# Optimization experiments

Hardware: AMD Instinct MI355X
Metric: run time of the kernel (lower is better)

The kernel has to match this reference:

```python
import jax, jax.numpy as jnp
import numpy as np

EPS = 1e-5
B, T, D, V, NB, C, R, MT = 2, 256, 2048, 32000, 4, 512, 32, 3


def ste_sign_vec(w):
    alpha = jnp.mean(jnp.abs(w))
    hard = alpha * jnp.sign(w)
    hard = jnp.where(hard == 0, alpha, hard)
    return w + jax.lax.stop_gradient(hard - w)


def ste_sign(w):
    alpha = jnp.mean(jnp.abs(w), axis=-1, keepdims=True)
    hard = alpha * jnp.sign(w)
    hard = jnp.where(hard == 0, alpha, hard)
    return w + jax.lax.stop_gradient(hard - w)


def layernorm(x, g, b):
    m = jnp.mean(x, axis=-1, keepdims=True)
    v = jnp.var(x, axis=-1, keepdims=True)
    return (x - m) * jax.lax.rsqrt(v + EPS) * g + b


def hdc_block(x, i, decay_logit, bv_q, bv_k, bv_v, rules, query_bind, logic_gate,
              ln_mem_g, ln_mem_b, ln_attn_g, ln_attn_b, ln_logic_g, ln_logic_b,
              ctrl_ln_g, ctrl_ln_b, down_w, down_b, up_w, up_b):
    t = jnp.arange(T)
    # --- EMA memory (conv1d with decay^k kernel == lower-tri decay matmul) ---
    decay = jax.nn.sigmoid(decay_logit[i])
    expnt = t[:, None] - t[None, :]                     # (T,T)
    A = jnp.where(expnt >= 0, decay ** jnp.maximum(expnt, 0).astype(x.dtype), 0.0)
    mem = jnp.einsum('ts,bsd->btd', A, x)
    x = layernorm(x + mem, ln_mem_g[i], ln_mem_b[i])
    # --- sigmoid-gated boolean causal attention ---
    Q = x * ste_sign_vec(bv_q[i])
    K = x * ste_sign_vec(bv_k[i])
    Vv = x * ste_sign_vec(bv_v[i])
    scores = jnp.einsum('btd,bsd->bts', Q, K) * (D ** -0.5)
    causal = t[:, None] >= t[None, :]
    attn = jnp.where(causal[None], jax.nn.sigmoid(scores * 4.0), 0.0)
    att_out = jnp.einsum('bts,bsd->btd', attn, Vv)
    x = layernorm(x + att_out, ln_attn_g[i], ln_attn_b[i])
    # --- logic layer: sum_r w_r * (x*rule_r) == x * (w @ rules) ---
    rls = ste_sign(rules[i])                            # (R,D)
    query = x * ste_sign_vec(query_bind[i])
    sim = jnp.einsum('btd,rd->btr', query, rls) * (D ** -0.5)
    rw = jax.nn.sigmoid(sim * 4.0)
    logic_out = x * jnp.einsum('btr,rd->btd', rw, rls)
    gate = jax.nn.sigmoid(logic_gate[i])
    x = layernorm(x + gate * (logic_out - x), ln_logic_g[i], ln_logic_b[i])
    # --- controller MLP (dropout inactive in eval) ---
    h = layernorm(x, ctrl_ln_g[i], ctrl_ln_b[i])
    h = jax.nn.gelu(h @ down_w[i].T + down_b[i], approximate=False)
    h = h @ up_w[i].T + up_b[i]
    return x + h


def setup_inputs() -> dict:
    key = jax.random.key(0)
    ks = jax.random.split(key, 12)
    nrm = jax.random.normal
    return {
        'idx': jax.random.randint(ks[0], (B, T), 0, V),
        'codebook': 0.02 * nrm(ks[1], (V, D)),
        'decay_logit': jnp.full((NB,), 2.0),
        'bv_q': 0.5 * nrm(ks[2], (NB, D)),
        'bv_k': 0.5 * nrm(ks[3], (NB, D)),
        'bv_v': 0.5 * nrm(ks[4], (NB, D)),
        'rules': 0.5 * nrm(ks[5], (NB, R, D)),
        'query_bind': 0.5 * nrm(ks[6], (NB, D)),
        'logic_gate': jnp.full((NB,), -1.0),
        'ln_mem_g': jnp.ones((NB, D)), 'ln_mem_b': jnp.zeros((NB, D)),
        'ln_attn_g': jnp.ones((NB, D)), 'ln_attn_b': jnp.zeros((NB, D)),
        'ln_logic_g': jnp.ones((NB, D)), 'ln_logic_b': jnp.zeros((NB, D)),
        'ctrl_ln_g': jnp.ones((NB, D)), 'ctrl_ln_b': jnp.zeros((NB, D)),
        'down_w': nrm(ks[7], (NB, C, D)) / np.sqrt(D), 'down_b': jnp.zeros((NB, C)),
        'up_w': nrm(ks[8], (NB, D, C)) / np.sqrt(C), 'up_b': jnp.zeros((NB, D)),
        'tl_gates': jnp.zeros((MT,)),
        'tl_pos': 0.01 * nrm(ks[9], (MT, D)),
        'tl_ln_g': jnp.ones((D,)), 'tl_ln_b': jnp.zeros((D,)),
        'out_ln_g': jnp.ones((D,)), 'out_ln_b': jnp.zeros((D,)),
        'output_scale': jnp.array(1.0),
    }


def reference(idx, codebook, decay_logit, bv_q, bv_k, bv_v, rules, query_bind,
              logic_gate, ln_mem_g, ln_mem_b, ln_attn_g, ln_attn_b, ln_logic_g,
              ln_logic_b, ctrl_ln_g, ctrl_ln_b, down_w, down_b, up_w, up_b,
              tl_gates, tl_pos, tl_ln_g, tl_ln_b, out_ln_g, out_ln_b, output_scale):
    blk = (decay_logit, bv_q, bv_k, bv_v, rules, query_bind, logic_gate,
           ln_mem_g, ln_mem_b, ln_attn_g, ln_attn_b, ln_logic_g, ln_logic_b,
           ctrl_ln_g, ctrl_ln_b, down_w, down_b, up_w, up_b)

    def run_blocks(h):
        for i in range(NB):
            h = hdc_block(h, i, *blk)
        return h

    # encode: STE bipolar codebook + cyclic permutation positional binding
    tokens = ste_sign(jnp.take(codebook, idx, axis=0))  # (B,T,D)
    perm = (jnp.arange(D)[None, :] - jnp.arange(T)[:, None]) % D  # (T,D)
    tokens = jnp.take_along_axis(tokens, jnp.broadcast_to(perm[None], tokens.shape), axis=2)

    h = run_blocks(tokens)
    for ti in range(1, MT):  # thought loop (n_thoughts = max_thoughts)
        gate = jax.nn.sigmoid(tl_gates[ti])
        thought = run_blocks(layernorm(h, tl_ln_g, tl_ln_b) + tl_pos[ti])
        h = h + gate * (thought - h)

    h = layernorm(h, out_ln_g, out_ln_b)
    logits = (h @ codebook.T) * output_scale  # (B,T,V) weight-tied decoder
    return logits
```

## Files before the change

kernel.cpp:

```cpp
#include <hip/hip_runtime.h>
#include <math.h>

#define TT   256
#define DD   2048
#define VV   32000
#define NBLK 4
#define CC   512
#define RR   32
#define MTT  3
#define NBAT 2
#define NTOK 512

typedef unsigned int u32;
typedef unsigned short ushort_t;
typedef __attribute__((ext_vector_type(8))) short s16x8;
typedef __attribute__((ext_vector_type(4))) float f32x4;

__device__ __forceinline__ float sigm(float x){ return 1.0f/(1.0f+expf(-x)); }

__device__ __forceinline__ ushort_t f2bf(float f){
  u32 u = __float_as_uint(f);
  u32 r = (u + 0x7fffu + ((u >> 16) & 1u)) >> 16;
  return (ushort_t)r;
}
__device__ __forceinline__ float bf2f(ushort_t u){
  return __uint_as_float(((u32)u) << 16);
}

__device__ __forceinline__ void async_copy16(void* lds, const void* g){
  __builtin_amdgcn_global_load_lds((const __attribute__((address_space(1))) u32*)g,
                                   (__attribute__((address_space(3))) u32*)lds, 16, 0, 0);
}

__device__ __forceinline__ float block_sum256(float v){
  #pragma unroll
  for (int off = 32; off > 0; off >>= 1) v += __shfl_down(v, off);
  __shared__ float sh[4];
  __syncthreads();
  if ((threadIdx.x & 63) == 0) sh[threadIdx.x >> 6] = v;
  __syncthreads();
  return sh[0] + sh[1] + sh[2] + sh[3];
}

__global__ __launch_bounds__(256) void cvt2_kernel(const float* __restrict__ a,
    ushort_t* __restrict__ oa, long na4,
    const float* __restrict__ b, ushort_t* __restrict__ ob, long nb4){
  long i = (long)blockIdx.x * 256 + threadIdx.x;
  long stride = (long)gridDim.x * 256;
  long tot = na4 + nb4;
  for (; i < tot; i += stride){
    const float* src = (i < na4) ? a : b;
    ushort_t* dst = (i < na4) ? oa : ob;
    long k = (i < na4) ? i : i - na4;
    float4 v = ((const float4*)src)[k];
    ushort4 o;
    o.x = f2bf(v.x); o.y = f2bf(v.y); o.z = f2bf(v.z); o.w = f2bf(v.w);
    ((ushort4*)dst)[k] = o;
  }
}

__global__ __launch_bounds__(256) void sign_prep_kernel(
    const float* __restrict__ bv_q, const float* __restrict__ bv_k,
    const float* __restrict__ bv_v, const float* __restrict__ query_bind,
    const float* __restrict__ rules,
    float* __restrict__ SQK, float* __restrict__ SV, float* __restrict__ SQB,
    ushort_t* __restrict__ RLSb){
  int b = blockIdx.x;
  if (b < NBLK){
    const float* q = bv_q + (size_t)b * DD;
    const float* k = bv_k + (size_t)b * DD;
    float sq = 0.f, sk = 0.f;
    #pragma unroll
    for (int j = 0; j < 8; j++){
      int d = threadIdx.x + j*256;
      sq += fabsf(q[d]); sk += fabsf(k[d]);
    }
    float aq = block_sum256(sq) * (1.f/DD);
    float ak = block_sum256(sk) * (1.f/DD);
    float a2 = aq * ak;
    float* o = SQK + (size_t)b * DD;
    #pragma unroll
    for (int j = 0; j < 8; j++){
      int d = threadIdx.x + j*256;
      o[d] = ((q[d] < 0.f) != (k[d] < 0.f)) ? -a2 : a2;
    }
    return;
  }
  const float* w; float* of = nullptr; ushort_t* ob = nullptr;
  if (b < 2*NBLK){ w = bv_v + (size_t)(b - NBLK) * DD; of = SV + (size_t)(b - NBLK) * DD; }
  else if (b < 3*NBLK){ w = query_bind + (size_t)(b - 2*NBLK) * DD; of = SQB + (size_t)(b - 2*NBLK) * DD; }
  else { int r = b - 3*NBLK; w = rules + (size_t)r * DD; ob = RLSb + (size_t)r * DD; }
  float s = 0.f;
  #pragma unroll
  for (int j = 0; j < 8; j++) s += fabsf(w[threadIdx.x + j*256]);
  float a = block_sum256(s) * (1.f/DD);
  #pragma unroll
  for (int j = 0; j < 8; j++){
    int d = threadIdx.x + j*256;
    float v = (w[d] < 0.f) ? -a : a;
    if (of) of[d] = v;
    else    ob[d] = f2bf(v);
  }
}

__global__ __launch_bounds__(256) void encode_kernel(const int* __restrict__ idx,
    const float* __restrict__ cb, float* __restrict__ X, ushort_t* __restrict__ Xrb){
  int token = blockIdx.x;
  int t = token & (TT - 1);
  size_t row = (size_t)idx[token] * DD;
  float s = 0.f;
  #pragma unroll
  for (int j = 0; j < 8; j++) s += fabsf(cb[row + threadIdx.x + j*256]);
  float a = block_sum256(s) * (1.f/DD);
  #pragma unroll
  for (int j = 0; j < 8; j++){
    int d = threadIdx.x + j*256;
    float w = cb[row + ((d - t) & (DD - 1))];
    float v = (w < 0.f) ? -a : a;
    X[(size_t)token * DD + d] = v;
    Xrb[(size_t)token * DD + d] = f2bf(v);
  }
}

__global__ __launch_bounds__(256) void adec_kernel(const float* __restrict__ decay_logit,
    ushort_t* __restrict__ Adec){
  int i = blockIdx.y, t = blockIdx.x, s = threadIdx.x;
  float decay = sigm(decay_logit[i]);
  float l2 = log2f(decay);
  int e = t - s;
  float v = (e < 0) ? 0.f : exp2f((float)e * l2);
  Adec[((size_t)i*TT + t)*TT + s] = f2bf(v);
}

__global__ __launch_bounds__(256) void ln_kernel(const float* __restrict__ A,
    const float* __restrict__ g, const float* __restrict__ be,
    float* __restrict__ out, ushort_t* __restrict__ outb,
    const float* __restrict__ qscale, ushort_t* __restrict__ outq,
    const float* __restrict__ vscale, ushort_t* __restrict__ outv){
  size_t row = blockIdx.x;
  const float* a = A + row * DD;
  float vals[8]; float s = 0.f, ss = 0.f;
  #pragma unroll
  for (int j = 0; j < 8; j++){
    int d = threadIdx.x + j*256;
    float v = a[d];
    vals[j] = v; s += v; ss += v*v;
  }
  float mean = block_sum256(s) * (1.f/DD);
  float var  = block_sum256(ss) * (1.f/DD) - mean*mean;
  float inv  = rsqrtf(var + 1e-5f);
  #pragma unroll
  for (int j = 0; j < 8; j++){
    int d = threadIdx.x + j*256;
    float y = (vals[j] - mean) * inv * g[d] + be[d];
    if (out)  out[row*DD + d] = y;
    if (outb) outb[row*DD + d] = f2bf(y);
    if (outq) outq[row*DD + d] = f2bf(y * qscale[d]);
    if (outv) outv[row*DD + d] = f2bf(y * vscale[d]);
  }
}

__global__ __launch_bounds__(256) void fuse_logic_kernel(const float* __restrict__ T0,
    const ushort_t* __restrict__ RLSi, const float* __restrict__ SQBi,
    const float* __restrict__ g2, const float* __restrict__ b2,
    const float* __restrict__ gate_ptr,
    const float* __restrict__ g3, const float* __restrict__ b3,
    const float* __restrict__ g4, const float* __restrict__ b4,
    float* __restrict__ X, ushort_t* __restrict__ T1b){
  __shared__ float sh[256*33];
  __shared__ float red[8*32];
  __shared__ float rwsh[32];
  const float RSD = 0.022097086912079608f;
  int tid = threadIdx.x;
  size_t tok = blockIdx.x;
  const float* a = T0 + tok * DD;
  float v[8]; float s = 0.f, ss = 0.f;
  #pragma unroll
  for (int j = 0; j < 8; j++){
    int d = tid + 256*j;
    v[j] = a[d]; s += v[j]; ss += v[j]*v[j];
  }
  float mean = block_sum256(s) * (1.f/DD);
  float var  = block_sum256(ss) * (1.f/DD) - mean*mean;
  float inv  = rsqrtf(var + 1e-5f);
  float y2[8], xq[8];
  #pragma unroll
  for (int j = 0; j < 8; j++){
    int d = tid + 256*j;
    y2[j] = (v[j] - mean) * inv * g2[d] + b2[d];
    xq[j] = y2[j] * SQBi[d];
  }
  float aa[32];
  #pragma unroll 4
  for (int r = 0; r < 32; r++){
    float t = 0.f;
    #pragma unroll
    for (int j = 0; j < 8; j++)
      t = fmaf(xq[j], bf2f(RLSi[(size_t)r*DD + tid + 256*j]), t);
    aa[r] = t;
  }
  #pragma unroll
  for (int r = 0; r < 32; r++) sh[tid*33 + r] = aa[r];
  __syncthreads();
  {
    int r = tid & 31, gg = tid >> 5;
    float t = 0.f;
    #pragma unroll 8
    for (int i = 0; i < 32; i++) t += sh[(gg*32 + i)*33 + r];
    red[gg*32 + r] = t;
  }
  __syncthreads();
  if (tid < 32){
    float t = 0.f;
    #pragma unroll
    for (int gg = 0; gg < 8; gg++) t += red[gg*32 + tid];
    rwsh[tid] = sigm(4.f * RSD * t);
  }
  __syncthreads();
  float gate = sigm(*gate_ptr);
  float p3[8]; s = 0.f; ss = 0.f;
  #pragma unroll
  for (int j = 0; j < 8; j++){
    int d = tid + 256*j;
    float t = 0.f;
    #pragma unroll 8
    for (int r = 0; r < 32; r++)
      t = fmaf(rwsh[r], bf2f(RLSi[(size_t)r*DD + d]), t);
    float lo = y2[j] * t;
    p3[j] = y2[j] + gate * (lo - y2[j]);
    s += p3[j]; ss += p3[j]*p3[j];
  }
  mean = block_sum256(s) * (1.f/DD);
  var  = block_sum256(ss) * (1.f/DD) - mean*mean;
  inv  = rsqrtf(var + 1e-5f);
  float y3[8]; s = 0.f; ss = 0.f;
  #pragma unroll
  for (int j = 0; j < 8; j++){
    int d = tid + 256*j;
    y3[j] = (p3[j] - mean) * inv * g3[d] + b3[d];
    X[tok*DD + d] = y3[j];
    s += y3[j]; ss += y3[j]*y3[j];
  }
  mean = block_sum256(s) * (1.f/DD);
  var  = block_sum256(ss) * (1.f/DD) - mean*mean;
  inv  = rsqrtf(var + 1e-5f);
  #pragma unroll
  for (int j = 0; j < 8; j++){
    int d = tid + 256*j;
    T1b[tok*DD + d] = f2bf((y3[j] - mean) * inv * g4[d] + b4[d]);
  }
}

__global__ __launch_bounds__(256) void tl_kernel(const float* __restrict__ Xr,
    float* __restrict__ H, const float* __restrict__ gate_ptr,
    const float* __restrict__ g, const float* __restrict__ be,
    const float* __restrict__ pos,
    float* __restrict__ outX, ushort_t* __restrict__ outXb){
  size_t row = blockIdx.x;
  float gate = gate_ptr ? sigm(*gate_ptr) : 1.f;
  float v[8]; float s = 0.f, ss = 0.f;
  #pragma unroll
  for (int j = 0; j < 8; j++){
    int d = threadIdx.x + j*256;
    float xr = Xr[row*DD + d];
    float hv = gate_ptr ? H[row*DD + d] : 0.f;
    float hn = gate_ptr ? (hv + gate * (xr - hv)) : xr;
    H[row*DD + d] = hn;
    v[j] = hn; s += hn; ss += hn*hn;
  }
  float mean = block_sum256(s) * (1.f/DD);
  float var  = block_sum256(ss) * (1.f/DD) - mean*mean;
  float inv  = rsqrtf(var + 1e-5f);
  #pragma unroll
  for (int j = 0; j < 8; j++){
    int d = threadIdx.x + j*256;
    float y = (v[j] - mean) * inv * g[d] + be[d];
    if (pos) y += pos[d];
    if (outX)  outX[row*DD + d] = y;
    if (outXb) outXb[row*DD + d] = f2bf(y);
  }
}

template<int BM, int BN, int SPLITK, int ACT, bool CAUSAL, bool OUTBF>
__global__ __launch_bounds__(256) void gemm_nt(const ushort_t* __restrict__ A,
    const ushort_t* __restrict__ B, void* __restrict__ Cv,
    int K, int lda, int ldb, int ldc,
    long sA, long sB, long sC,
    const float* __restrict__ colscale, const float* __restrict__ bias,
    const float* __restrict__ res, ushort_t* __restrict__ mirror,
    const float* __restrict__ alpha_ptr, float alpha_c)
{
  constexpr int FM = BM / 32;
  constexpr int FN = BN / 32;
  __shared__ __align__(16) ushort_t shA[BM * 64];
  __shared__ __align__(16) ushort_t shB[BN * 64];
  const int tid = threadIdx.x;
  const int l = tid & 63, w = tid >> 6;
  const int wr = w >> 1, wc = w & 1;
  const int row0 = blockIdx.y * BM, col0 = blockIdx.x * BN;
  const int zb = blockIdx.z / SPLITK, zk = blockIdx.z % SPLITK;

  if (CAUSAL && col0 > row0 + BM - 1) return;

  A += (size_t)zb * sA;
  B += (size_t)zb * sB;
  const int kbeg = zk * (K / SPLITK), kend = kbeg + K / SPLITK;

  f32x4 acc[FM][FN] = {};

  for (int kt = kbeg; kt < kend; kt += 64){
    #pragma unroll
    for (int i = 0; i < BM/32; i++){
      int o = i*4096 + tid*16;
      int r = o >> 7, c = (o >> 4) & 7;
      int lc = c ^ (r & 7);
      async_copy16((char*)shA + o, A + (size_t)(row0 + r) * lda + kt + lc*8);
    }
    #pragma unroll
    for (int i = 0; i < BN/32; i++){
      int o = i*4096 + tid*16;
      int r = o >> 7, c = (o >> 4) & 7;
      int lc = c ^ (r & 7);
      async_copy16((char*)shB + o, B + (size_t)(col0 + r) * ldb + kt + lc*8);
    }
    __syncthreads();
    #pragma unroll
    for (int kk = 0; kk < 2; kk++){
      s16x8 af[FM], bfr[FN];
      #pragma unroll
      for (int mi = 0; mi < FM; mi++){
        int r = wr*(BM/2) + mi*16 + (l & 15);
        int c = kk*4 + (l >> 4);
        af[mi] = *(const s16x8*)((const char*)shA + r*128 + (c ^ (r & 7))*16);
      }
      #pragma unroll
      for (int ni = 0; ni < FN; ni++){
        int r = wc*(BN/2) + ni*16 + (l & 15);
        int c = kk*4 + (l >> 4);
        bfr[ni] = *(const s16x8*)((const char*)shB + r*128 + (c ^ (r & 7))*16);
      }
      #pragma unroll
      for (int mi = 0; mi < FM; mi++)
        #pragma unroll
        for (int ni = 0; ni < FN; ni++)
          acc[mi][ni] = __builtin_amdgcn_mfma_f32_16x16x32_bf16(af[mi], bfr[ni], acc[mi][ni], 0, 0, 0);
    }
    __syncthreads();
  }

  if (SPLITK > 1){
    float* P = (float*)Cv + (size_t)blockIdx.z * sC;
    #pragma unroll
    for (int mi = 0; mi < FM; mi++)
      #pragma unroll
      for (int ni = 0; ni < FN; ni++)
        #pragma unroll
        for (int j = 0; j < 4; j++){
          int m = row0 + wr*(BM/2) + mi*16 + (l >> 4)*4 + j;
          int n = col0 + wc*(BN/2) + ni*16 + (l & 15);
          P[(size_t)m * ldc + n] = acc[mi][ni][j];
        }
    return;
  }

  float alpha = alpha_c * (alpha_ptr ? *alpha_ptr : 1.f);
  float* Cf = (float*)Cv + (size_t)zb * sC;
  ushort_t* Cb = (ushort_t*)Cv + (size_t)zb * sC;
  const float* resz = res ? res + (size_t)zb * sC : nullptr;
  #pragma unroll
  for (int mi = 0; mi < FM; mi++){
    #pragma unroll
    for (int ni = 0; ni < FN; ni++){
      #pragma unroll
      for (int j = 0; j < 4; j++){
        int m = row0 + wr*(BM/2) + mi*16 + (l >> 4)*4 + j;
        int n = col0 + wc*(BN/2) + ni*16 + (l & 15);
        float v = acc[mi][ni][j] * alpha;
        if (colscale) v *= colscale[n];
        if (bias) v += bias[n];
        if (ACT == 1) v = sigm(4.f * v);
        else if (ACT == 2) v = 0.5f * v * (1.f + erff(v * 0.70710678118654752f));
        if (CAUSAL && n > m) v = 0.f;
        if (resz) v += resz[(size_t)m * ldc + n];
        if (OUTBF) Cb[(size_t)m * ldc + n] = f2bf(v);
        else       Cf[(size_t)m * ldc + n] = v;
        if (mirror) mirror[(size_t)m * ldc + n] = f2bf(v);
      }
    }
  }
}

__global__ __launch_bounds__(256) void gemm_nn(const ushort_t* __restrict__ A,
    const ushort_t* __restrict__ B, float* __restrict__ C,
    int K, int lda, int ldb, int ldc,
    long sA, long sB, long sC,
    const float* __restrict__ res)
{
  __shared__ __align__(16) ushort_t shA[64 * 64];
  __shared__ __align__(16) ushort_t shB[64 * 64];
  const int tid = threadIdx.x;
  const int l = tid & 63, w = tid >> 6;
  const int wr = w >> 1, wc = w & 1;
  const int row0 = blockIdx.y * 64, col0 = blockIdx.x * 64;
  A += (size_t)blockIdx.z * sA;
  B += (size_t)blockIdx.z * sB;

  const int kb = tid & 63;
  const int nb0 = (tid >> 6) * 8;

  f32x4 acc[2][2] = {};

  for (int kt = 0; kt < K; kt += 64){
    #pragma unroll
    for (int i = 0; i < 2; i++){
      int o = i*4096 + tid*16;
      int r = o >> 7, c = (o >> 4) & 7;
      int lc = c ^ (r & 7);
      async_copy16((char*)shA + o, A + (size_t)(row0 + r) * lda + kt + lc*8);
    }
    #pragma unroll
    for (int i = 0; i < 2; i++){
      int n0 = nb0 + i*32;
      s16x8 v = *(const s16x8*)(B + (size_t)(kt + kb) * ldb + col0 + n0);
      #pragma unroll
      for (int j = 0; j < 8; j++){
        int n = n0 + j;
        int off = n*128 + (((kb >> 3) ^ (n & 7)) << 4) + ((kb & 7) << 1);
        *(ushort_t*)((char*)shB + off) = (ushort_t)v[j];
      }
    }
    __syncthreads();
    #pragma unroll
    for (int kk = 0; kk < 2; kk++){
      s16x8 af[2], bfr[2];
      #pragma unroll
      for (int mi = 0; mi < 2; mi++){
        int r = wr*32 + mi*16 + (l & 15);
        int c = kk*4 + (l >> 4);
        af[mi] = *(const s16x8*)((const char*)shA + r*128 + ((c ^ (r & 7)) << 4));
      }
      #pragma unroll
      for (int ni = 0; ni < 2; ni++){
        int r = wc*32 + ni*16 + (l & 15);
        int c = kk*4 + (l >> 4);
        bfr[ni] = *(const s16x8*)((const char*)shB + r*128 + ((c ^ (r & 7)) << 4));
      }
      #pragma unroll
      for (int mi = 0; mi < 2; mi++)
        #pragma unroll
        for (int ni = 0; ni < 2; ni++)
          acc[mi][ni] = __builtin_amdgcn_mfma_f32_16x16x32_bf16(af[mi], bfr[ni], acc[mi][ni], 0, 0, 0);
    }
    __syncthreads();
  }

  float* Cf = C + (size_t)blockIdx.z * sC;
  const float* resz = res ? res + (size_t)blockIdx.z * sC : nullptr;
  #pragma unroll
  for (int mi = 0; mi < 2; mi++)
    #pragma unroll
    for (int ni = 0; ni < 2; ni++)
      #pragma unroll
      for (int j = 0; j < 4; j++){
        int m = row0 + wr*32 + mi*16 + (l >> 4)*4 + j;
        int n = col0 + wc*32 + ni*16 + (l & 15);
        float v = acc[mi][ni][j];
        if (resz) v += resz[(size_t)m * ldc + n];
        Cf[(size_t)m * ldc + n] = v;
      }
}

__global__ __launch_bounds__(256) void gemm_ntf(const ushort_t* __restrict__ A,
    const float* __restrict__ B, float* __restrict__ C,
    int K, int lda, int ldb, int ldc,
    const float* __restrict__ alpha_ptr)
{
  constexpr int BM = 256, BN = 64, FM = 8, FN = 2;
  __shared__ __align__(16) ushort_t shA[BM * 64];
  __shared__ __align__(16) ushort_t shB[BN * 64];
  const int tid = threadIdx.x;
  const int l = tid & 63, w = tid >> 6;
  const int wr = w >> 1, wc = w & 1;
  const int row0 = blockIdx.y * BM, col0 = blockIdx.x * BN;

  f32x4 acc[FM][FN] = {};

  for (int kt = 0; kt < K; kt += 64){
    #pragma unroll
    for (int i = 0; i < BM/32; i++){
      int o = i*4096 + tid*16;
      int r = o >> 7, c = (o >> 4) & 7;
      int lc = c ^ (r & 7);
      async_copy16((char*)shA + o, A + (size_t)(row0 + r) * lda + kt + lc*8);
    }
    #pragma unroll
    for (int i = 0; i < 4; i++){
      int c2 = tid + i*256;
      int r = c2 & 63, kq = c2 >> 6;
      float4 v = *(const float4*)(B + (size_t)(col0 + r) * ldb + kt + kq*4);
      u32 p0 = ((u32)f2bf(v.y) << 16) | (u32)f2bf(v.x);
      u32 p1 = ((u32)f2bf(v.w) << 16) | (u32)f2bf(v.z);
      int off = r*128 + (((kq >> 1) ^ (r & 7)) << 4) + ((kq & 1) << 3);
      uint2 pp; pp.x = p0; pp.y = p1;
      *(uint2*)((char*)shB + off) = pp;
    }
    __syncthreads();
    #pragma unroll
    for (int kk = 0; kk < 2; kk++){
      s16x8 af[FM], bfr[FN];
      #pragma unroll
      for (int mi = 0; mi < FM; mi++){
        int r = wr*(BM/2) + mi*16 + (l & 15);
        int c = kk*4 + (l >> 4);
        af[mi] = *(const s16x8*)((const char*)shA + r*128 + ((c ^ (r & 7)) << 4));
      }
      #pragma unroll
      for (int ni = 0; ni < FN; ni++){
        int r = wc*(BN/2) + ni*16 + (l & 15);
        int c = kk*4 + (l >> 4);
        bfr[ni] = *(const s16x8*)((const char*)shB + r*128 + ((c ^ (r & 7)) << 4));
      }
      #pragma unroll
      for (int mi = 0; mi < FM; mi++)
        #pragma unroll
        for (int ni = 0; ni < FN; ni++)
          acc[mi][ni] = __builtin_amdgcn_mfma_f32_16x16x32_bf16(af[mi], bfr[ni], acc[mi][ni], 0, 0, 0);
    }
    __syncthreads();
  }

  float alpha = *alpha_ptr;
  #pragma unroll
  for (int mi = 0; mi < FM; mi++)
    #pragma unroll
    for (int ni = 0; ni < FN; ni++)
      #pragma unroll
      for (int j = 0; j < 4; j++){
        int m = row0 + wr*(BM/2) + mi*16 + (l >> 4)*4 + j;
        int n = col0 + wc*(BN/2) + ni*16 + (l & 15);
        C[(size_t)m * ldc + n] = acc[mi][ni][j] * alpha;
      }
}

template<int S, int ACT, bool CAUSAL, bool OUTBF>
__global__ __launch_bounds__(256) void reduce_epi(const float* __restrict__ P,
    void* __restrict__ outv, int M, int N, const float* __restrict__ bias, float alpha){
  long MN = (long)M * N;
  long idx = ((long)blockIdx.x * 256 + threadIdx.x) * 4;
  int b = (int)(idx / MN);
  long r = idx - (long)b * MN;
  int m = (int)(r / N), n = (int)(r % N);
  float vv[4] = {0.f, 0.f, 0.f, 0.f};
  #pragma unroll
  for (int s = 0; s < S; s++){
    float4 p = *(const float4*)&P[((long)(b*S + s)) * MN + r];
    vv[0] += p.x; vv[1] += p.y; vv[2] += p.z; vv[3] += p.w;
  }
  ushort4 ob; float4 of;
  float* po = (float*)&of;
  ushort_t* pb = (ushort_t*)&ob;
  #pragma unroll
  for (int j = 0; j < 4; j++){
    float v = vv[j] * alpha;
    if (bias) v += bias[n + j];
    if (ACT == 1) v = sigm(4.f * v);
    else if (ACT == 2) v = 0.5f * v * (1.f + erff(v * 0.70710678118654752f));
    if (CAUSAL && n + j > m) v = 0.f;
    po[j] = v; pb[j] = f2bf(v);
  }
  if (OUTBF) *(ushort4*)&((ushort_t*)outv)[(long)b*MN + r] = ob;
  else       *(float4*)&((float*)outv)[(long)b*MN + r] = of;
}

extern "C" void kernel_launch(void* const* d_in, const int* in_sizes, int n_in,
                              void* d_out, int out_size, void* d_ws, size_t ws_size,
                              hipStream_t stream){
  const int*   idx        = (const int*)  d_in[0];
  const float* cb         = (const float*)d_in[1];
  const float* decay_lg   = (const float*)d_in[2];
  const float* bv_q       = (const float*)d_in[3];
  const float* bv_k       = (const float*)d_in[4];
  const float* bv_v       = (const float*)d_in[5];
  const float* rules      = (const float*)d_in[6];
  const float* query_bind = (const float*)d_in[7];
  const float* logic_gate = (const float*)d_in[8];
  const float* ln_mem_g   = (const float*)d_in[9];
  const float* ln_mem_b   = (const float*)d_in[10];
  const float* ln_attn_g  = (const float*)d_in[11];
  const float* ln_attn_b  = (const float*)d_in[12];
  const float* ln_logic_g = (const float*)d_in[13];
  const float* ln_logic_b = (const float*)d_in[14];
  const float* ctrl_g     = (const float*)d_in[15];
  const float* ctrl_b     = (const float*)d_in[16];
  const float* down_w     = (const float*)d_in[17];
  const float* down_b     = (const float*)d_in[18];
  const float* up_w       = (const float*)d_in[19];
  const float* up_b       = (const float*)d_in[20];
  const float* tl_gates   = (const float*)d_in[21];
  const float* tl_pos     = (const float*)d_in[22];
  const float* tl_g       = (const float*)d_in[23];
  const float* tl_b       = (const float*)d_in[24];
  const float* out_g      = (const float*)d_in[25];
  const float* out_b      = (const float*)d_in[26];
  const float* oscale     = (const float*)d_in[27];
  float* out = (float*)d_out;

  const size_t ND = (size_t)NTOK * DD;
  char* p = (char*)d_ws;
  auto alloc = [&](size_t bytes){ void* r = p; p += (bytes + 255) & ~(size_t)255; return r; };
  float*    X       = (float*)   alloc(ND * 4);
  float*    H       = (float*)   alloc(ND * 4);
  float*    T0      = (float*)   alloc(ND * 4);
  ushort_t* Xrb     = (ushort_t*)alloc(ND * 2);
  ushort_t* Xb      = (ushort_t*)alloc(ND * 2);
  ushort_t* Xqb     = (ushort_t*)alloc(ND * 2);
  ushort_t* Xvb     = (ushort_t*)alloc(ND * 2);
  ushort_t* T1b     = (ushort_t*)alloc(ND * 2);
  ushort_t* ATTNb   = (ushort_t*)alloc((size_t)NBAT * TT * TT * 2);
  ushort_t* CBb     = (ushort_t*)alloc((size_t)NTOK * CC * 2);
  float*    PP      = (float*)   alloc((size_t)8 * NTOK * CC * 4);
  float*    SQK     = (float*)   alloc((size_t)NBLK * DD * 4);
  float*    SV      = (float*)   alloc((size_t)NBLK * DD * 4);
  float*    SQB     = (float*)   alloc((size_t)NBLK * DD * 4);
  ushort_t* RLSb    = (ushort_t*)alloc((size_t)NBLK * RR * DD * 2);
  ushort_t* Adec    = (ushort_t*)alloc((size_t)NBLK * TT * TT * 2);
  ushort_t* down_wb = (ushort_t*)alloc((size_t)NBLK * CC * DD * 2);
  ushort_t* up_wb   = (ushort_t*)alloc((size_t)NBLK * DD * CC * 2);

  const float RSD = 0.022097086912079608f;

  sign_prep_kernel<<<3*NBLK + NBLK*RR, 256, 0, stream>>>(
      bv_q, bv_k, bv_v, query_bind, rules, SQK, SV, SQB, RLSb);
  adec_kernel<<<dim3(TT, NBLK), 256, 0, stream>>>(decay_lg, Adec);
  cvt2_kernel<<<2048, 256, 0, stream>>>(down_w, down_wb, (long)NBLK*CC*DD/4,
                                        up_w, up_wb, (long)NBLK*DD*CC/4);
  encode_kernel<<<NTOK, 256, 0, stream>>>(idx, cb, X, Xrb);

  auto run_blocks = [&](){
    for (int i = 0; i < NBLK; i++){
      const size_t iD = (size_t)i * DD;
      gemm_nn<<<dim3(DD/64, TT/64, NBAT), 256, 0, stream>>>(
          Adec + (size_t)i*TT*TT, Xrb, T0, TT, TT, DD, DD,
          0, (long)TT*DD, (long)TT*DD, X);
      ln_kernel<<<NTOK, 256, 0, stream>>>(T0, ln_mem_g + iD, ln_mem_b + iD,
          X, Xb, SQK + iD, Xqb, SV + iD, Xvb);
      gemm_nt<64,64,8,0,true,false><<<dim3(TT/64, TT/64, NBAT*8), 256, 0, stream>>>(
          Xqb, Xb, PP, DD, DD, DD, TT,
          (long)TT*DD, (long)TT*DD, (long)TT*TT,
          nullptr, nullptr, nullptr, nullptr, nullptr, 1.f);
      reduce_epi<8,1,true,true><<<(NBAT*TT*TT)/1024, 256, 0, stream>>>(
          PP, ATTNb, TT, TT, nullptr, RSD);
      gemm_nn<<<dim3(DD/64, TT/64, NBAT), 256, 0, stream>>>(
          ATTNb, Xvb, T0, TT, TT, DD, DD,
          (long)TT*TT, (long)TT*DD, (long)TT*DD, X);
      fuse_logic_kernel<<<NTOK, 256, 0, stream>>>(T0,
          RLSb + (size_t)i*RR*DD, SQB + iD,
          ln_attn_g + iD, ln_attn_b + iD, logic_gate + i,
          ln_logic_g + iD, ln_logic_b + iD, ctrl_g + iD, ctrl_b + iD,
          X, T1b);
      gemm_nt<64,64,8,0,false,false><<<dim3(CC/64, NTOK/64, 8), 256, 0, stream>>>(
          T1b, down_wb + (size_t)i*CC*DD, PP, DD, DD, DD, CC,
          0, 0, (long)NTOK*CC,
          nullptr, nullptr, nullptr, nullptr, nullptr, 1.f);
      reduce_epi<8,2,false,true><<<(NTOK*CC)/1024, 256, 0, stream>>>(
          PP, CBb, NTOK, CC, down_b + (size_t)i*CC, 1.f);
      gemm_nt<64,64,1,0,false,false><<<dim3(DD/64, NTOK/64, 1), 256, 0, stream>>>(
          CBb, up_wb + (size_t)i*DD*CC, X, CC, CC, CC, DD,
          0, 0, 0, nullptr, up_b + iD, X, Xrb, nullptr, 1.f);
    }
  };

  run_blocks();
  tl_kernel<<<NTOK, 256, 0, stream>>>(X, H, nullptr, tl_g, tl_b,
      tl_pos + (size_t)1*DD, X, Xrb);
  run_blocks();
  tl_kernel<<<NTOK, 256, 0, stream>>>(X, H, tl_gates + 1, tl_g, tl_b,
      tl_pos + (size_t)2*DD, X, Xrb);
  run_blocks();
  tl_kernel<<<NTOK, 256, 0, stream>>>(X, H, tl_gates + 2, out_g, out_b,
      nullptr, nullptr, T1b);
  gemm_ntf<<<dim3(VV/64, NTOK/256, 1), 256, 0, stream>>>(
      T1b, cb, out, DD, DD, DD, VV, oscale);
}
```

Baseline: 1.248 ms.

## Double-buffer LDS tiles in GEMM kernels and merge decay-matrix prep into sign prep

The gemm_nt and gemm_ntf kernels now keep two shared-memory buffers and issue the loads for the next K tile while MFMAs run on the current one. In gemm_ntf the fp32 B operand is prefetched into registers and converted and written to LDS after compute. This targets the global-load latency that was exposed by the old load-sync-compute loop. The cost is double the LDS per block, which can lower occupancy, most notably for the 256-row gemm_ntf tile. Separately, the decay-matrix kernel is folded into sign_prep_kernel, removing one launch.

```diff
diff --git a/kernel.cpp b/kernel.cpp
--- a/kernel.cpp
+++ b/kernel.cpp
@@ -62,10 +62,20 @@
 __global__ __launch_bounds__(256) void sign_prep_kernel(
     const float* __restrict__ bv_q, const float* __restrict__ bv_k,
     const float* __restrict__ bv_v, const float* __restrict__ query_bind,
-    const float* __restrict__ rules,
+    const float* __restrict__ rules, const float* __restrict__ decay_logit,
     float* __restrict__ SQK, float* __restrict__ SV, float* __restrict__ SQB,
-    ushort_t* __restrict__ RLSb){
+    ushort_t* __restrict__ RLSb, ushort_t* __restrict__ Adec){
   int b = blockIdx.x;
+  if (b >= 3*NBLK + NBLK*RR){
+    int e = b - (3*NBLK + NBLK*RR);
+    int i = e >> 8, t = e & (TT - 1), s = threadIdx.x;
+    float decay = sigm(decay_logit[i]);
+    float l2 = log2f(decay);
+    int ex = t - s;
+    float v = (ex < 0) ? 0.f : exp2f((float)ex * l2);
+    Adec[((size_t)i*TT + t)*TT + s] = f2bf(v);
+    return;
+  }
   if (b < NBLK){
     const float* q = bv_q + (size_t)b * DD;
     const float* k = bv_k + (size_t)b * DD;
@@ -120,16 +130,6 @@
     X[(size_t)token * DD + d] = v;
     Xrb[(size_t)token * DD + d] = f2bf(v);
   }
-}
-
-__global__ __launch_bounds__(256) void adec_kernel(const float* __restrict__ decay_logit,
-    ushort_t* __restrict__ Adec){
-  int i = blockIdx.y, t = blockIdx.x, s = threadIdx.x;
-  float decay = sigm(decay_logit[i]);
-  float l2 = log2f(decay);
-  int e = t - s;
-  float v = (e < 0) ? 0.f : exp2f((float)e * l2);
-  Adec[((size_t)i*TT + t)*TT + s] = f2bf(v);
 }
 
 __global__ __launch_bounds__(256) void ln_kernel(const float* __restrict__ A,
@@ -292,8 +292,8 @@
 {
   constexpr int FM = BM / 32;
   constexpr int FN = BN / 32;
-  __shared__ __align__(16) ushort_t shA[BM * 64];
-  __shared__ __align__(16) ushort_t shB[BN * 64];
+  __shared__ __align__(16) ushort_t shA[2][BM * 64];
+  __shared__ __align__(16) ushort_t shB[2][BN * 64];
   const int tid = threadIdx.x;
   const int l = tid & 63, w = tid >> 6;
   const int wr = w >> 1, wc = w & 1;
@@ -306,24 +306,30 @@
   B += (size_t)zb * sB;
   const int kbeg = zk * (K / SPLITK), kend = kbeg + K / SPLITK;
 
-  f32x4 acc[FM][FN] = {};
-
-  for (int kt = kbeg; kt < kend; kt += 64){
+  auto stage = [&](int buf, int kt){
     #pragma unroll
     for (int i = 0; i < BM/32; i++){
       int o = i*4096 + tid*16;
       int r = o >> 7, c = (o >> 4) & 7;
       int lc = c ^ (r & 7);
-      async_copy16((char*)shA + o, A + (size_t)(row0 + r) * lda + kt + lc*8);
+      async_copy16((char*)shA[buf] + o, A + (size_t)(row0 + r) * lda + kt + lc*8);
     }
     #pragma unroll
     for (int i = 0; i < BN/32; i++){
       int o = i*4096 + tid*16;
       int r = o >> 7, c = (o >> 4) & 7;
       int lc = c ^ (r & 7);
-      async_copy16((char*)shB + o, B + (size_t)(col0 + r) * ldb + kt + lc*8);
-    }
-    __syncthreads();
+      async_copy16((char*)shB[buf] + o, B + (size_t)(col0 + r) * ldb + kt + lc*8);
+    }
+  };
+
+  f32x4 acc[FM][FN] = {};
+
+  stage(0, kbeg);
+  __syncthreads();
+  for (int kt = kbeg; kt < kend; kt += 64){
+    int cur = ((kt - kbeg) >> 6) & 1, nxt = cur ^ 1;
+    if (kt + 64 < kend) stage(nxt, kt + 64);
     #pragma unroll
     for (int kk = 0; kk < 2; kk++){
       s16x8 af[FM], bfr[FN];
@@ -331,13 +337,13 @@
       for (int mi = 0; mi < FM; mi++){
         int r = wr*(BM/2) + mi*16 + (l & 15);
         int c = kk*4 + (l >> 4);
-        af[mi] = *(const s16x8*)((const char*)shA + r*128 + (c ^ (r & 7))*16);
+        af[mi] = *(const s16x8*)((const char*)shA[cur] + r*128 + ((c ^ (r & 7)) << 4));
       }
       #pragma unroll
       for (int ni = 0; ni < FN; ni++){
         int r = wc*(BN/2) + ni*16 + (l & 15);
         int c = kk*4 + (l >> 4);
-        bfr[ni] = *(const s16x8*)((const char*)shB + r*128 + (c ^ (r & 7))*16);
+        bfr[ni] = *(const s16x8*)((const char*)shB[cur] + r*128 + ((c ^ (r & 7)) << 4));
       }
       #pragma unroll
       for (int mi = 0; mi < FM; mi++)
@@ -476,35 +482,57 @@
     const float* __restrict__ alpha_ptr)
 {
   constexpr int BM = 256, BN = 64, FM = 8, FN = 2;
-  __shared__ __align__(16) ushort_t shA[BM * 64];
-  __shared__ __align__(16) ushort_t shB[BN * 64];
+  __shared__ __align__(16) ushort_t shA[2][BM * 64];
+  __shared__ __align__(16) ushort_t shB[2][BN * 64];
   const int tid = threadIdx.x;
   const int l = tid & 63, w = tid >> 6;
   const int wr = w >> 1, wc = w & 1;
   const int row0 = blockIdx.y * BM, col0 = blockIdx.x * BN;
 
-  f32x4 acc[FM][FN] = {};
-
-  for (int kt = 0; kt < K; kt += 64){
-    #pragma unroll
-    for (int i = 0; i < BM/32; i++){
+  auto stageA = [&](int buf, int kt){
+    #pragma unroll
+    for (int i = 0; i < FM; i++){
       int o = i*4096 + tid*16;
       int r = o >> 7, c = (o >> 4) & 7;
       int lc = c ^ (r & 7);
-      async_copy16((char*)shA + o, A + (size_t)(row0 + r) * lda + kt + lc*8);
-    }
+      async_copy16((char*)shA[buf] + o, A + (size_t)(row0 + r) * lda + kt + lc*8);
+    }
+  };
+  auto loadB = [&](float4* bre, int kt){
     #pragma unroll
     for (int i = 0; i < 4; i++){
-      int c2 = tid + i*256;
-      int r = c2 & 63, kq = c2 >> 6;
-      float4 v = *(const float4*)(B + (size_t)(col0 + r) * ldb + kt + kq*4);
+      int c2 = tid + i*256, r = c2 & 63, kq = c2 >> 6;
+      bre[i] = *(const float4*)(B + (size_t)(col0 + r) * ldb + kt + kq*4);
+    }
+  };
+  auto writeB = [&](int buf, const float4* bre){
+    #pragma unroll
+    for (int i = 0; i < 4; i++){
+      int c2 = tid + i*256, r = c2 & 63, kq = c2 >> 6;
+      float4 v = bre[i];
       u32 p0 = ((u32)f2bf(v.y) << 16) | (u32)f2bf(v.x);
       u32 p1 = ((u32)f2bf(v.w) << 16) | (u32)f2bf(v.z);
       int off = r*128 + (((kq >> 1) ^ (r & 7)) << 4) + ((kq & 1) << 3);
       uint2 pp; pp.x = p0; pp.y = p1;
-      *(uint2*)((char*)shB + off) = pp;
-    }
-    __syncthreads();
+      *(uint2*)((char*)shB[buf] + off) = pp;
+    }
+  };
+
+  f32x4 acc[FM][FN] = {};
+  float4 bre[4];
+
+  loadB(bre, 0);
+  stageA(0, 0);
+  writeB(0, bre);
+  __syncthreads();
+
+  for (int kt = 0; kt < K; kt += 64){
+    int cur = (kt >> 6) & 1, nxt = cur ^ 1;
+    bool more = (kt + 64 < K);
+    if (more){
+      loadB(bre, kt + 64);
+      stageA(nxt, kt + 64);
+    }
     #pragma unroll
     for (int kk = 0; kk < 2; kk++){
       s16x8 af[FM], bfr[FN];
@@ -512,13 +540,13 @@
       for (int mi = 0; mi < FM; mi++){
         int r = wr*(BM/2) + mi*16 + (l & 15);
         int c = kk*4 + (l >> 4);
-        af[mi] = *(const s16x8*)((const char*)shA + r*128 + ((c ^ (r & 7)) << 4));
+        af[mi] = *(const s16x8*)((const char*)shA[cur] + r*128 + ((c ^ (r & 7)) << 4));
       }
       #pragma unroll
       for (int ni = 0; ni < FN; ni++){
         int r = wc*(BN/2) + ni*16 + (l & 15);
         int c = kk*4 + (l >> 4);
-        bfr[ni] = *(const s16x8*)((const char*)shB + r*128 + ((c ^ (r & 7)) << 4));
+        bfr[ni] = *(const s16x8*)((const char*)shB[cur] + r*128 + ((c ^ (r & 7)) << 4));
       }
       #pragma unroll
       for (int mi = 0; mi < FM; mi++)
@@ -526,6 +554,7 @@
         for (int ni = 0; ni < FN; ni++)
           acc[mi][ni] = __builtin_amdgcn_mfma_f32_16x16x32_bf16(af[mi], bfr[ni], acc[mi][ni], 0, 0, 0);
     }
+    if (more) writeB(nxt, bre);
     __syncthreads();
   }
 
@@ -629,9 +658,8 @@
 
   const float RSD = 0.022097086912079608f;
 
-  sign_prep_kernel<<<3*NBLK + NBLK*RR, 256, 0, stream>>>(
-      bv_q, bv_k, bv_v, query_bind, rules, SQK, SV, SQB, RLSb);
-  adec_kernel<<<dim3(TT, NBLK), 256, 0, stream>>>(decay_lg, Adec);
+  sign_prep_kernel<<<3*NBLK + NBLK*RR + NBLK*TT, 256, 0, stream>>>(
+      bv_q, bv_k, bv_v, query_bind, rules, decay_lg, SQK, SV, SQB, RLSb, Adec);
   cvt2_kernel<<<2048, 256, 0, stream>>>(down_w, down_wb, (long)NBLK*CC*DD/4,
                                         up_w, up_wb, (long)NBLK*DD*CC/4);
   encode_kernel<<<NTOK, 256, 0, stream>>>(idx, cb, X, Xrb);
```

Result: no change. 1.260 ms (+1.0%).

## Pre-convert codebook to bf16 and use tiled bf16 GEMM for logits

Applied to the files above, without the earlier changes.

Replaces the output projection kernel, which converted the fp32 codebook to bf16 inside its K-loop, with a separate bulk conversion pass into workspace followed by the generic 128x128 bf16 gemm_nt. The bf16 codebook buffer aliases the start of the workspace, where X and H live; those buffers are dead by then, and T1b is moved past the aliased region. The decay-matrix kernel is also folded into sign_prep_kernel to save a launch. The trade is an extra full pass over the codebook (fp32 read plus bf16 write) against cheaper B-tile loads and a larger output tile. It also needs a larger workspace and depends on the buffer aliasing being correct.

```diff
diff --git a/kernel.cpp b/kernel.cpp
--- a/kernel.cpp
+++ b/kernel.cpp
@@ -59,13 +59,35 @@
   }
 }
 
+__global__ __launch_bounds__(256) void cvt_bf16_kernel(const float* __restrict__ in,
+    ushort_t* __restrict__ out, long n4){
+  long i = (long)blockIdx.x * 256 + threadIdx.x;
+  long stride = (long)gridDim.x * 256;
+  for (; i < n4; i += stride){
+    float4 v = ((const float4*)in)[i];
+    ushort4 o;
+    o.x = f2bf(v.x); o.y = f2bf(v.y); o.z = f2bf(v.z); o.w = f2bf(v.w);
+    ((ushort4*)out)[i] = o;
+  }
+}
+
 __global__ __launch_bounds__(256) void sign_prep_kernel(
     const float* __restrict__ bv_q, const float* __restrict__ bv_k,
     const float* __restrict__ bv_v, const float* __restrict__ query_bind,
-    const float* __restrict__ rules,
+    const float* __restrict__ rules, const float* __restrict__ decay_logit,
     float* __restrict__ SQK, float* __restrict__ SV, float* __restrict__ SQB,
-    ushort_t* __restrict__ RLSb){
+    ushort_t* __restrict__ RLSb, ushort_t* __restrict__ Adec){
   int b = blockIdx.x;
+  if (b >= 3*NBLK + NBLK*RR){
+    int e = b - (3*NBLK + NBLK*RR);
+    int i = e >> 8, t = e & (TT - 1), s = threadIdx.x;
+    float decay = sigm(decay_logit[i]);
+    float l2 = log2f(decay);
+    int ex = t - s;
+    float v = (ex < 0) ? 0.f : exp2f((float)ex * l2);
+    Adec[((size_t)i*TT + t)*TT + s] = f2bf(v);
+    return;
+  }
   if (b < NBLK){
     const float* q = bv_q + (size_t)b * DD;
     const float* k = bv_k + (size_t)b * DD;
@@ -120,16 +142,6 @@
     X[(size_t)token * DD + d] = v;
     Xrb[(size_t)token * DD + d] = f2bf(v);
   }
-}
-
-__global__ __launch_bounds__(256) void adec_kernel(const float* __restrict__ decay_logit,
-    ushort_t* __restrict__ Adec){
-  int i = blockIdx.y, t = blockIdx.x, s = threadIdx.x;
-  float decay = sigm(decay_logit[i]);
-  float l2 = log2f(decay);
-  int e = t - s;
-  float v = (e < 0) ? 0.f : exp2f((float)e * l2);
-  Adec[((size_t)i*TT + t)*TT + s] = f2bf(v);
 }
 
 __global__ __launch_bounds__(256) void ln_kernel(const float* __restrict__ A,
@@ -331,13 +343,13 @@
       for (int mi = 0; mi < FM; mi++){
         int r = wr*(BM/2) + mi*16 + (l & 15);
         int c = kk*4 + (l >> 4);
-        af[mi] = *(const s16x8*)((const char*)shA + r*128 + (c ^ (r & 7))*16);
+        af[mi] = *(const s16x8*)((const char*)shA + r*128 + ((c ^ (r & 7)) << 4));
       }
       #pragma unroll
       for (int ni = 0; ni < FN; ni++){
         int r = wc*(BN/2) + ni*16 + (l & 15);
         int c = kk*4 + (l >> 4);
-        bfr[ni] = *(const s16x8*)((const char*)shB + r*128 + (c ^ (r & 7))*16);
+        bfr[ni] = *(const s16x8*)((const char*)shB + r*128 + ((c ^ (r & 7)) << 4));
       }
       #pragma unroll
       for (int mi = 0; mi < FM; mi++)
@@ -467,78 +479,6 @@
         float v = acc[mi][ni][j];
         if (resz) v += resz[(size_t)m * ldc + n];
         Cf[(size_t)m * ldc + n] = v;
-      }
-}
-
-__global__ __launch_bounds__(256) void gemm_ntf(const ushort_t* __restrict__ A,
-    const float* __restrict__ B, float* __restrict__ C,
-    int K, int lda, int ldb, int ldc,
-    const float* __restrict__ alpha_ptr)
-{
-  constexpr int BM = 256, BN = 64, FM = 8, FN = 2;
-  __shared__ __align__(16) ushort_t shA[BM * 64];
-  __shared__ __align__(16) ushort_t shB[BN * 64];
-  const int tid = threadIdx.x;
-  const int l = tid & 63, w = tid >> 6;
-  const int wr = w >> 1, wc = w & 1;
-  const int row0 = blockIdx.y * BM, col0 = blockIdx.x * BN;
-
-  f32x4 acc[FM][FN] = {};
-
-  for (int kt = 0; kt < K; kt += 64){
-    #pragma unroll
-    for (int i = 0; i < BM/32; i++){
-      int o = i*4096 + tid*16;
-      int r = o >> 7, c = (o >> 4) & 7;
-      int lc = c ^ (r & 7);
-      async_copy16((char*)shA + o, A + (size_t)(row0 + r) * lda + kt + lc*8);
-    }
-    #pragma unroll
-    for (int i = 0; i < 4; i++){
-      int c2 = tid + i*256;
-      int r = c2 & 63, kq = c2 >> 6;
-      float4 v = *(const float4*)(B + (size_t)(col0 + r) * ldb + kt + kq*4);
-      u32 p0 = ((u32)f2bf(v.y) << 16) | (u32)f2bf(v.x);
-      u32 p1 = ((u32)f2bf(v.w) << 16) | (u32)f2bf(v.z);
-      int off = r*128 + (((kq >> 1) ^ (r & 7)) << 4) + ((kq & 1) << 3);
-      uint2 pp; pp.x = p0; pp.y = p1;
-      *(uint2*)((char*)shB + off) = pp;
-    }
-    __syncthreads();
-    #pragma unroll
-    for (int kk = 0; kk < 2; kk++){
-      s16x8 af[FM], bfr[FN];
-      #pragma unroll
-      for (int mi = 0; mi < FM; mi++){
-        int r = wr*(BM/2) + mi*16 + (l & 15);
-        int c = kk*4 + (l >> 4);
-        af[mi] = *(const s16x8*)((const char*)shA + r*128 + ((c ^ (r & 7)) << 4));
-      }
-      #pragma unroll
-      for (int ni = 0; ni < FN; ni++){
-        int r = wc*(BN/2) + ni*16 + (l & 15);
-        int c = kk*4 + (l >> 4);
-        bfr[ni] = *(const s16x8*)((const char*)shB + r*128 + ((c ^ (r & 7)) << 4));
-      }
-      #pragma unroll
-      for (int mi = 0; mi < FM; mi++)
-        #pragma unroll
-        for (int ni = 0; ni < FN; ni++)
-          acc[mi][ni] = __builtin_amdgcn_mfma_f32_16x16x32_bf16(af[mi], bfr[ni], acc[mi][ni], 0, 0, 0);
-    }
-    __syncthreads();
-  }
-
-  float alpha = *alpha_ptr;
-  #pragma unroll
-  for (int mi = 0; mi < FM; mi++)
-    #pragma unroll
-    for (int ni = 0; ni < FN; ni++)
-      #pragma unroll
-      for (int j = 0; j < 4; j++){
-        int m = row0 + wr*(BM/2) + mi*16 + (l >> 4)*4 + j;
-        int n = col0 + wc*(BN/2) + ni*16 + (l & 15);
-        C[(size_t)m * ldc + n] = acc[mi][ni][j] * alpha;
       }
 }
 
@@ -606,7 +546,10 @@
   float* out = (float*)d_out;
 
   const size_t ND = (size_t)NTOK * DD;
-  char* p = (char*)d_ws;
+  const size_t CBB = (size_t)VV * DD * 2;
+  char* base = (char*)d_ws;
+  ushort_t* cb_b = (ushort_t*)base;
+  char* p = base;
   auto alloc = [&](size_t bytes){ void* r = p; p += (bytes + 255) & ~(size_t)255; return r; };
   float*    X       = (float*)   alloc(ND * 4);
   float*    H       = (float*)   alloc(ND * 4);
@@ -615,9 +558,8 @@
   ushort_t* Xb      = (ushort_t*)alloc(ND * 2);
   ushort_t* Xqb     = (ushort_t*)alloc(ND * 2);
   ushort_t* Xvb     = (ushort_t*)alloc(ND * 2);
-  ushort_t* T1b     = (ushort_t*)alloc(ND * 2);
   ushort_t* ATTNb   = (ushort_t*)alloc((size_t)NBAT * TT * TT * 2);
-  ushort_t* CBb     = (ushort_t*)alloc((size_t)NTOK * CC * 2);
+  ushort_t* CBbuf   = (ushort_t*)alloc((size_t)NTOK * CC * 2);
   float*    PP      = (float*)   alloc((size_t)8 * NTOK * CC * 4);
   float*    SQK     = (float*)   alloc((size_t)NBLK * DD * 4);
   float*    SV      = (float*)   alloc((size_t)NBLK * DD * 4);
@@ -626,12 +568,12 @@
   ushort_t* Adec    = (ushort_t*)alloc((size_t)NBLK * TT * TT * 2);
   ushort_t* down_wb = (ushort_t*)alloc((size_t)NBLK * CC * DD * 2);
   ushort_t* up_wb   = (ushort_t*)alloc((size_t)NBLK * DD * CC * 2);
+  ushort_t* T1b = (ushort_t*)(base + CBB);
 
   const float RSD = 0.022097086912079608f;
 
-  sign_prep_kernel<<<3*NBLK + NBLK*RR, 256, 0, stream>>>(
-      bv_q, bv_k, bv_v, query_bind, rules, SQK, SV, SQB, RLSb);
-  adec_kernel<<<dim3(TT, NBLK), 256, 0, stream>>>(decay_lg, Adec);
+  sign_prep_kernel<<<3*NBLK + NBLK*RR + NBLK*TT, 256, 0, stream>>>(
+      bv_q, bv_k, bv_v, query_bind, rules, decay_lg, SQK, SV, SQB, RLSb, Adec);
   cvt2_kernel<<<2048, 256, 0, stream>>>(down_w, down_wb, (long)NBLK*CC*DD/4,
                                         up_w, up_wb, (long)NBLK*DD*CC/4);
   encode_kernel<<<NTOK, 256, 0, stream>>>(idx, cb, X, Xrb);
@@ -663,9 +605,9 @@
           0, 0, (long)NTOK*CC,
           nullptr, nullptr, nullptr, nullptr, nullptr, 1.f);
       reduce_epi<8,2,false,true><<<(NTOK*CC)/1024, 256, 0, stream>>>(
-          PP, CBb, NTOK, CC, down_b + (size_t)i*CC, 1.f);
+          PP, CBbuf, NTOK, CC, down_b + (size_t)i*CC, 1.f);
       gemm_nt<64,64,1,0,false,false><<<dim3(DD/64, NTOK/64, 1), 256, 0, stream>>>(
-          CBb, up_wb + (size_t)i*DD*CC, X, CC, CC, CC, DD,
+          CBbuf, up_wb + (size_t)i*DD*CC, X, CC, CC, CC, DD,
           0, 0, 0, nullptr, up_b + iD, X, Xrb, nullptr, 1.f);
     }
   };
@@ -679,6 +621,8 @@
   run_blocks();
   tl_kernel<<<NTOK, 256, 0, stream>>>(X, H, tl_gates + 2, out_g, out_b,
       nullptr, nullptr, T1b);
-  gemm_ntf<<<dim3(VV/64, NTOK/256, 1), 256, 0, stream>>>(
-      T1b, cb, out, DD, DD, DD, VV, oscale);
-}
+  cvt_bf16_kernel<<<4096, 256, 0, stream>>>(cb, cb_b, (long)VV*DD/4);
+  gemm_nt<128,128,1,0,false,false><<<dim3(VV/128, NTOK/128, 1), 256, 0, stream>>>(
+      T1b, cb_b, out, DD, DD, DD, VV,
+      0, 0, 0, nullptr, nullptr, nullptr, nullptr, oscale, 1.f);
+}
```

Result: no change. 1.245 ms (-0.2%).
